# Kernel tuning notes

Measured on AMD Instinct MI355X. Metric: run time of the kernel, lower is better.

The kernel has to match this reference:

```python
import jax, jax.numpy as jnp
import numpy as np

B, H, W, DIM = 8, 64, 64, 256
HEADS, DH = 8, 64
HID = HEADS * DH  # 512
EPS = 1e-5


def setup_inputs() -> dict:
    key = jax.random.key(0)
    k0, k1, k2 = jax.random.split(key, 3)
    return {
        "x": jax.random.normal(k0, (B, H, W, DIM), dtype=jnp.float32),
        "w_qkv": jax.random.normal(k1, (DIM, 3 * HID), dtype=jnp.float32) / np.sqrt(DIM),
        "gn_scale": jnp.ones((HID,), jnp.float32),
        "gn_bias": jnp.zeros((HID,), jnp.float32),
        "w_out": jax.random.normal(k2, (HID, DIM), dtype=jnp.float32) / np.sqrt(HID),
        "b_out": jnp.zeros((DIM,), jnp.float32),
    }


def reference(x, w_qkv, gn_scale, gn_bias, w_out, b_out):
    b, h, w, c = x.shape
    n = h * w
    scale = DH ** -0.5
    # 1x1 conv (no bias) == channel matmul
    qkv = jnp.einsum('bxyc,cf->bxyf', x, w_qkv)
    q, k, v = jnp.split(qkv, 3, axis=-1)
    # 'b x y (h c) -> b h c (x y)'
    to_heads = lambda t: t.reshape(b, n, HEADS, DH).transpose(0, 2, 3, 1)
    q, k, v = map(to_heads, (q, k, v))  # [b, heads, d, n]
    q = jax.nn.softmax(q, axis=-2) * scale  # softmax over feature dim d
    k = jax.nn.softmax(k, axis=-1)          # softmax over token dim n
    context = jnp.einsum('bhdn,bhen->bhde', k, v)   # small d x e context
    out = jnp.einsum('bhde,bhdn->bhen', context, q)  # [b, heads, e, n]
    # 'b h c (x y) -> b x y (h c)'
    out = out.transpose(0, 3, 1, 2).reshape(b, h, w, HID)
    # GroupNorm with 1 group: normalize over (H, W, C) per sample
    mu = out.mean(axis=(1, 2, 3), keepdims=True)
    var = out.var(axis=(1, 2, 3), keepdims=True)
    out = (out - mu) * jax.lax.rsqrt(var + EPS) * gn_scale + gn_bias
    # final 1x1 conv with bias
    return jnp.einsum('bxyf,fc->bxyc', out, w_out) + b_out
```

## Files before the change

### kernel.cpp

```cpp
#include <hip/hip_runtime.h>


typedef unsigned short ushort_t;
typedef __attribute__((ext_vector_type(8))) short short8;
typedef __attribute__((ext_vector_type(4))) float floatx4;

__device__ __forceinline__ float b2f(ushort_t u) {
  unsigned int i = ((unsigned int)u) << 16;
  float f;
  __builtin_memcpy(&f, &i, 4);
  return f;
}
__device__ __forceinline__ ushort_t f2b(float f) {
  unsigned int i;
  __builtin_memcpy(&i, &f, 4);
  unsigned int r = (i + 0x7FFFu + ((i >> 16) & 1u)) >> 16;
  return (ushort_t)r;
}

__device__ __forceinline__ void load_lds16(const ushort_t* g, ushort_t* l) {
  __builtin_amdgcn_global_load_lds(
      (const __attribute__((address_space(1))) unsigned int*)g,
      (__attribute__((address_space(3))) unsigned int*)l, 16, 0, 0);
}

__global__ __launch_bounds__(256) void cast_f32_bf16(
    const float* __restrict__ in, ushort_t* __restrict__ out) {
  long i = ((long)blockIdx.x * 256 + threadIdx.x) * 4;
  float4 v = *(const float4*)(in + i);
  ushort4 o;
  o.x = f2b(v.x);
  o.y = f2b(v.y);
  o.z = f2b(v.z);
  o.w = f2b(v.w);
  *(ushort4*)(out + i) = o;
}

__global__ __launch_bounds__(256) void transpose_f32_bf16(
    const float* __restrict__ in, ushort_t* __restrict__ out, int R, int C,
    const float* __restrict__ scale) {
  __shared__ ushort_t t[32][33];
  int c0 = blockIdx.x * 32, r0 = blockIdx.y * 32;
  int tx = threadIdx.x & 31, ty = threadIdx.x >> 5;
  for (int i = 0; i < 32; i += 8) {
    float s = scale ? scale[r0 + ty + i] : 1.0f;
    t[ty + i][tx] = f2b(in[(long)(r0 + ty + i) * C + c0 + tx] * s);
  }
  __syncthreads();
  for (int i = 0; i < 32; i += 8)
    out[(long)(c0 + ty + i) * R + r0 + tx] = t[tx][ty + i];
}

__global__ __launch_bounds__(64) void prep_gw_kernel(
    const float* __restrict__ gn_scale, const float* __restrict__ gn_bias,
    const float* __restrict__ w_out, const float* __restrict__ b_out,
    float* __restrict__ gw1, float* __restrict__ bias2) {
  int c = blockIdx.x * 64 + threadIdx.x;
  float g1 = 0.f, b2 = 0.f;
  for (int f = 0; f < 512; ++f) {
    float w = w_out[f * 256 + c];
    g1 += gn_scale[f] * w;
    b2 += gn_bias[f] * w;
  }
  gw1[c] = g1;
  bias2[c] = b2 + b_out[c];
}

template <int MODE, bool SWAP>
__global__ __launch_bounds__(256) void gemm_tpl(
    const ushort_t* __restrict__ A, const ushort_t* __restrict__ Bt,
    void* __restrict__ Cv, int M, int K, int F,
    const float* __restrict__ murs, const float* __restrict__ gw1,
    const float* __restrict__ bias2) {
  __shared__ __align__(16) ushort_t As[128][32];
  __shared__ __align__(16) ushort_t Bs[128][32];
  int tid = threadIdx.x;
  long m0 = (long)(SWAP ? blockIdx.y : blockIdx.x) * 128;
  long f0 = (long)(SWAP ? blockIdx.x : blockIdx.y) * 128;
  int wv = tid >> 6, lane = tid & 63;
  int wm = wv & 1, wf = wv >> 1;
  int l15 = lane & 15, quad = lane >> 4;

  floatx4 acc[4][4];
  floatx4 zero = {0.f, 0.f, 0.f, 0.f};
  for (int i = 0; i < 4; i++)
    for (int j = 0; j < 4; j++) acc[i][j] = zero;

  for (int k0 = 0; k0 < K; k0 += 32) {
    __syncthreads();
#pragma unroll
    for (int r = 0; r < 2; ++r) {
      int chunk = r * 256 + tid;
      int row = chunk >> 2;
      int kc = chunk & 3;
      load_lds16(A + (m0 + row) * (long)K + k0 + kc * 8, &As[row][kc * 8]);
      load_lds16(Bt + (f0 + row) * (long)K + k0 + kc * 8, &Bs[row][kc * 8]);
    }
    __syncthreads();
    short8 af[4], bfr[4];
#pragma unroll
    for (int mt = 0; mt < 4; mt++)
      af[mt] = *(const short8*)(&As[wm * 64 + mt * 16 + l15][quad * 8]);
#pragma unroll
    for (int ft = 0; ft < 4; ft++)
      bfr[ft] = *(const short8*)(&Bs[wf * 64 + ft * 16 + l15][quad * 8]);
#pragma unroll
    for (int mt = 0; mt < 4; mt++)
#pragma unroll
      for (int ft = 0; ft < 4; ft++)
        acc[mt][ft] = __builtin_amdgcn_mfma_f32_16x16x32_bf16(
            af[mt], bfr[ft], acc[mt][ft], 0, 0, 0);
  }

  if constexpr (MODE == 0) {
    ushort_t* C = (ushort_t*)Cv;
#pragma unroll
    for (int mt = 0; mt < 4; mt++)
#pragma unroll
      for (int ft = 0; ft < 4; ft++) {
        long col = f0 + wf * 64 + ft * 16 + l15;
#pragma unroll
        for (int r = 0; r < 4; r++) {
          long row = m0 + wm * 64 + mt * 16 + quad * 4 + r;
          C[row * F + col] = f2b(acc[mt][ft][r]);
        }
      }
  } else if constexpr (MODE == 1) {
    ushort_t* C = (ushort_t*)Cv;
    bool isk = (m0 < 512);
#pragma unroll
    for (int mt = 0; mt < 4; mt++)
#pragma unroll
      for (int ft = 0; ft < 4; ft++) {
        long col = f0 + wf * 64 + ft * 16 + l15;
#pragma unroll
        for (int r = 0; r < 4; r++) {
          long row = m0 + wm * 64 + mt * 16 + quad * 4 + r;
          float v = acc[mt][ft][r];
          if (isk) v = __expf(v);
          C[row * F + col] = f2b(v);
        }
      }
  } else {
    float* C = (float*)Cv;
    int b = (int)(m0 >> 12);
    float mu = murs[b * 2], rs = murs[b * 2 + 1];
#pragma unroll
    for (int mt = 0; mt < 4; mt++)
#pragma unroll
      for (int ft = 0; ft < 4; ft++) {
        long col = f0 + wf * 64 + ft * 16 + l15;
        float c1 = bias2[col] - rs * mu * gw1[col];
#pragma unroll
        for (int r = 0; r < 4; r++) {
          long row = m0 + wm * 64 + mt * 16 + quad * 4 + r;
          C[row * F + col] = rs * acc[mt][ft][r] + c1;
        }
      }
  }
}

__global__ __launch_bounds__(256) void ctx_mfma(
    const ushort_t* __restrict__ kvT, float* __restrict__ ctxP,
    float* __restrict__ ksumP) {
  int bh = blockIdx.x, cy = blockIdx.y;
  int b = bh >> 3, h = bh & 7;
  int tid = threadIdx.x, wv = tid >> 6, lane = tid & 63;
  int l15 = lane & 15, quad = lane >> 4;
  __shared__ __align__(16) ushort_t kTs[64 * 128];
  __shared__ __align__(16) ushort_t vTs[64 * 128];
  const ushort_t* kbase = kvT + (long)(h * 64) * 32768 + b * 4096 + cy * 256;
  const ushort_t* vbase = kbase + (long)512 * 32768;

  floatx4 acc[4], acc1;
  floatx4 zero = {0.f, 0.f, 0.f, 0.f};
  for (int i = 0; i < 4; i++) acc[i] = zero;
  acc1 = zero;
  short8 ones;
#pragma unroll
  for (int u = 0; u < 8; ++u) ones[u] = (short)0x3F80;

  int r4 = lane >> 4, c = lane & 15;
  for (int tile = 0; tile < 2; ++tile) {
    __syncthreads();
#pragma unroll
    for (int i = 0; i < 4; ++i) {
      int row = wv * 16 + i * 4 + r4;
      int gc = (c & 8) | ((c ^ row) & 7);
      load_lds16(kbase + (long)row * 32768 + tile * 128 + gc * 8,
                 kTs + (wv * 16 + i * 4) * 128 + lane * 8);
      load_lds16(vbase + (long)row * 32768 + tile * 128 + gc * 8,
                 vTs + (wv * 16 + i * 4) * 128 + lane * 8);
    }
    __syncthreads();
#pragma unroll
    for (int ks = 0; ks < 4; ++ks) {
      int d = wv * 16 + l15;
      int cidx = ks * 4 + quad;
      int sa = (cidx & 8) | ((cidx ^ d) & 7);
      short8 a = *(const short8*)(kTs + d * 128 + sa * 8);
      short8 bf[4];
#pragma unroll
      for (int ft = 0; ft < 4; ++ft) {
        int e = ft * 16 + l15;
        int sb = (cidx & 8) | ((cidx ^ e) & 7);
        bf[ft] = *(const short8*)(vTs + e * 128 + sb * 8);
      }
#pragma unroll
      for (int ft = 0; ft < 4; ++ft)
        acc[ft] = __builtin_amdgcn_mfma_f32_16x16x32_bf16(a, bf[ft], acc[ft],
                                                          0, 0, 0);
      acc1 = __builtin_amdgcn_mfma_f32_16x16x32_bf16(a, ones, acc1, 0, 0, 0);
    }
  }
  float* cb = ctxP + ((long)cy * 64 + bh) * 4096;
#pragma unroll
  for (int ft = 0; ft < 4; ++ft)
#pragma unroll
    for (int r = 0; r < 4; ++r)
      cb[(ft * 16 + l15) * 64 + wv * 16 + quad * 4 + r] = acc[ft][r];
  if (l15 == 0) {
    float* kb = ksumP + ((long)cy * 64 + bh) * 64;
#pragma unroll
    for (int r = 0; r < 4; ++r) kb[wv * 16 + quad * 4 + r] = acc1[r];
  }
}

__global__ __launch_bounds__(256) void reduce_kernel(
    const float* __restrict__ ctxP, const float* __restrict__ ksumP,
    ushort_t* __restrict__ ctxB) {
  int bid = blockIdx.x;
  int bh = bid >> 4;
  int j = (bid & 15) * 256 + threadIdx.x;
  int e = j >> 6, d = j & 63;
  float ks = 0.f;
#pragma unroll
  for (int c = 0; c < 16; ++c) ks += ksumP[((long)c * 64 + bh) * 64 + d];
  float s = 0.f;
#pragma unroll
  for (int c = 0; c < 16; ++c) s += ctxP[((long)c * 64 + bh) * 4096 + j];
  int slot = (d >> 3) ^ (e & 7);
  ctxB[(long)bh * 4096 + e * 64 + slot * 8 + (d & 7)] = f2b(s / ks);
}

__global__ __launch_bounds__(256) void qp_gemm_kernel(
    const ushort_t* __restrict__ q, const ushort_t* __restrict__ ctxB,
    ushort_t* __restrict__ A2, float* __restrict__ gstats) {
  int bh = blockIdx.x, chunk = blockIdx.y;
  int b = bh >> 3, h = bh & 7;
  int tid = threadIdx.x, wv = tid >> 6, lane = tid & 63;
  int l15 = lane & 15, quad = lane >> 4;
  __shared__ __align__(16) ushort_t As[128 * 64];
  __shared__ __align__(16) ushort_t Bs[64 * 64];
  __shared__ float rs[128];
  __shared__ float red[4][2];

  long rowbase = (long)b * 4096 + chunk * 128;

  {
    int tl = lane >> 3;
    int c = lane & 7;
    int j = c ^ tl;
    const ushort_t* g = q + (rowbase + wv * 32 + tl) * 512 + h * 64 + j * 8;
#pragma unroll
    for (int i = 0; i < 4; ++i)
      load_lds16(g + (long)i * 8 * 512, As + (wv * 32 + i * 8) * 64 + lane * 8);
  }
  {
#pragma unroll
    for (int i = 0; i < 2; ++i)
      load_lds16(ctxB + (long)bh * 4096 + (wv * 2 + i) * 512 + lane * 8,
                 Bs + (wv * 2 + i) * 512 + lane * 8);
  }
  __syncthreads();

  {
    int t = tid >> 1, half = tid & 1;
    ushort_t* row = As + t * 64;
    float s = 0.f;
#pragma unroll
    for (int i = 0; i < 4; ++i) {
      int slot = half * 4 + ((i + t) & 3);
      short8 vq = *(const short8*)(row + slot * 8);
      short8 eo;
#pragma unroll
      for (int u = 0; u < 8; ++u) {
        float e = __expf(b2f((ushort_t)vq[u]));
        s += e;
        eo[u] = (short)f2b(e);
      }
      *(short8*)(row + slot * 8) = eo;
    }
    s += __shfl_xor(s, 1);
    if (half == 0) rs[t] = 0.125f / s;
  }
  __syncthreads();

  floatx4 acc[2][4];
  floatx4 zero = {0.f, 0.f, 0.f, 0.f};
  for (int i = 0; i < 2; i++)
    for (int j = 0; j < 4; j++) acc[i][j] = zero;
#pragma unroll
  for (int k0 = 0; k0 < 2; ++k0) {
    short8 af[2], bfr[4];
#pragma unroll
    for (int mt = 0; mt < 2; mt++) {
      int row = wv * 32 + mt * 16 + l15;
      int slot = (k0 * 4 + quad) ^ (row & 7);
      af[mt] = *(const short8*)(As + row * 64 + slot * 8);
    }
#pragma unroll
    for (int ft = 0; ft < 4; ft++) {
      int e = ft * 16 + l15;
      int slot = (k0 * 4 + quad) ^ (e & 7);
      bfr[ft] = *(const short8*)(Bs + e * 64 + slot * 8);
    }
#pragma unroll
    for (int mt = 0; mt < 2; mt++)
#pragma unroll
      for (int ft = 0; ft < 4; ft++)
        acc[mt][ft] = __builtin_amdgcn_mfma_f32_16x16x32_bf16(
            af[mt], bfr[ft], acc[mt][ft], 0, 0, 0);
  }

  float lsum = 0.f, lss = 0.f;
#pragma unroll
  for (int mt = 0; mt < 2; mt++) {
    float rsv[4];
#pragma unroll
    for (int r = 0; r < 4; r++)
      rsv[r] = rs[wv * 32 + mt * 16 + quad * 4 + r];
#pragma unroll
    for (int ft = 0; ft < 4; ft++) {
      int col = h * 64 + ft * 16 + l15;
#pragma unroll
      for (int r = 0; r < 4; r++) {
        long row = rowbase + wv * 32 + mt * 16 + quad * 4 + r;
        float v = acc[mt][ft][r] * rsv[r];
        A2[row * 512 + col] = f2b(v);
        lsum += v;
        lss += v * v;
      }
    }
  }
  for (int o = 32; o > 0; o >>= 1) {
    lsum += __shfl_xor(lsum, o);
    lss += __shfl_xor(lss, o);
  }
  if (lane == 0) {
    red[wv][0] = lsum;
    red[wv][1] = lss;
  }
  __syncthreads();
  if (tid == 0) {
    float a = 0.f, c = 0.f;
    for (int w2 = 0; w2 < 4; w2++) {
      a += red[w2][0];
      c += red[w2][1];
    }
    atomicAdd(&gstats[b * 2], a);
    atomicAdd(&gstats[b * 2 + 1], c);
  }
}

__global__ __launch_bounds__(64) void finalize_murs(
    const float* __restrict__ gstats, float* __restrict__ murs) {
  int tid = threadIdx.x;
  if (tid < 8) {
    float cnt = 4096.f * 512.f;
    float mu = gstats[tid * 2] / cnt;
    float var = gstats[tid * 2 + 1] / cnt - mu * mu;
    murs[tid * 2] = mu;
    murs[tid * 2 + 1] = rsqrtf(var + 1e-5f);
  }
}

extern "C" void kernel_launch(void* const* d_in, const int* in_sizes, int n_in,
                              void* d_out, int out_size, void* d_ws,
                              size_t ws_size, hipStream_t stream) {
  const float* x = (const float*)d_in[0];
  const float* w_qkv = (const float*)d_in[1];
  const float* gn_scale = (const float*)d_in[2];
  const float* gn_bias = (const float*)d_in[3];
  const float* w_out = (const float*)d_in[4];
  const float* b_out = (const float*)d_in[5];
  float* out = (float*)d_out;

  char* w = (char*)d_ws;
  ushort_t* q = (ushort_t*)(w + 0);
  ushort_t* kvT = (ushort_t*)(w + 33554432);
  ushort_t* A2 = (ushort_t*)(w + 100663296);
  float* ctxP = (float*)(w + 134217728);
  float* ksumP = (float*)(w + 150994944);
  ushort_t* xb = (ushort_t*)(w + 167772160);
  ushort_t* wqkvT = (ushort_t*)(w + 184549376);
  ushort_t* w2T = (ushort_t*)(w + 185335808);
  ushort_t* ctxB = (ushort_t*)(w + 185630720);
  float* gstats = (float*)(w + 186679296);
  float* murs = (float*)(w + 186695744);
  float* bias2 = (float*)(w + 186695808);
  float* gw1 = (float*)(w + 186696832);

  hipMemsetAsync(gstats, 0, 64, stream);

  cast_f32_bf16<<<8388608 / 4 / 256, 256, 0, stream>>>(x, xb);
  transpose_f32_bf16<<<dim3(1536 / 32, 256 / 32), 256, 0, stream>>>(
      w_qkv, wqkvT, 256, 1536, nullptr);
  transpose_f32_bf16<<<dim3(256 / 32, 512 / 32), 256, 0, stream>>>(
      w_out, w2T, 512, 256, gn_scale);
  prep_gw_kernel<<<4, 64, 0, stream>>>(gn_scale, gn_bias, w_out, b_out, gw1,
                                       bias2);
  gemm_tpl<0, false><<<dim3(256, 4), 256, 0, stream>>>(
      xb, wqkvT, q, 32768, 256, 512, nullptr, nullptr, nullptr);
  gemm_tpl<1, true><<<dim3(256, 8), 256, 0, stream>>>(
      wqkvT + 512 * 256, xb, kvT, 1024, 256, 32768, nullptr, nullptr, nullptr);
  ctx_mfma<<<dim3(64, 16), 256, 0, stream>>>(kvT, ctxP, ksumP);
  reduce_kernel<<<1024, 256, 0, stream>>>(ctxP, ksumP, ctxB);
  qp_gemm_kernel<<<dim3(64, 32), 256, 0, stream>>>(q, ctxB, A2, gstats);
  finalize_murs<<<1, 64, 0, stream>>>(gstats, murs);
  gemm_tpl<2, false><<<dim3(256, 2), 256, 0, stream>>>(
      A2, w2T, out, 32768, 512, 256, murs, gw1, bias2);
}
```

Before: 270.5 us.

## Fuse Q projection GEMM with softmax and context multiply into one kernel

Removes the separate Q projection GEMM and its bf16 round trip through global memory. A new kernel computes the Q tile from xb and the Q weights, applies exp and the per-head softmax normalisation in registers, stages the probabilities in LDS, and multiplies by the per-head context. It also accumulates the GroupNorm statistics. This saves writing and re-reading a 32 MB intermediate and one launch, at the cost of higher LDS use (about 48 KB) and register pressure, which may lower occupancy.

```diff
diff --git a/kernel.cpp b/kernel.cpp
--- a/kernel.cpp
+++ b/kernel.cpp
@@ -112,20 +112,7 @@
             af[mt], bfr[ft], acc[mt][ft], 0, 0, 0);
   }
 
-  if constexpr (MODE == 0) {
-    ushort_t* C = (ushort_t*)Cv;
-#pragma unroll
-    for (int mt = 0; mt < 4; mt++)
-#pragma unroll
-      for (int ft = 0; ft < 4; ft++) {
-        long col = f0 + wf * 64 + ft * 16 + l15;
-#pragma unroll
-        for (int r = 0; r < 4; r++) {
-          long row = m0 + wm * 64 + mt * 16 + quad * 4 + r;
-          C[row * F + col] = f2b(acc[mt][ft][r]);
-        }
-      }
-  } else if constexpr (MODE == 1) {
+  if constexpr (MODE == 1) {
     ushort_t* C = (ushort_t*)Cv;
     bool isk = (m0 < 512);
 #pragma unroll
@@ -243,120 +230,171 @@
   ctxB[(long)bh * 4096 + e * 64 + slot * 8 + (d & 7)] = f2b(s / ks);
 }
 
-__global__ __launch_bounds__(256) void qp_gemm_kernel(
-    const ushort_t* __restrict__ q, const ushort_t* __restrict__ ctxB,
-    ushort_t* __restrict__ A2, float* __restrict__ gstats) {
-  int bh = blockIdx.x, chunk = blockIdx.y;
-  int b = bh >> 3, h = bh & 7;
-  int tid = threadIdx.x, wv = tid >> 6, lane = tid & 63;
+__global__ __launch_bounds__(256) void qattn_kernel(
+    const ushort_t* __restrict__ xb, const ushort_t* __restrict__ wqT,
+    const ushort_t* __restrict__ ctxB, ushort_t* __restrict__ A2,
+    float* __restrict__ gstats) {
+  __shared__ __align__(16) char lds[49216];
+  ushort_t* As = (ushort_t*)lds;
+  ushort_t* Bs = (ushort_t*)(lds + 8192);
+  ushort_t* P = (ushort_t*)lds;
+  ushort_t* Cs = (ushort_t*)(lds + 32768);
+  float* red = (float*)(lds + 49152);
+
+  int tid = threadIdx.x;
+  int bx = blockIdx.x, by = blockIdx.y;
+  long m0 = (long)bx * 128;
+  long f0 = (long)by * 128;
+  int wv = tid >> 6, lane = tid & 63;
+  int wm = wv & 1, wf = wv >> 1;
   int l15 = lane & 15, quad = lane >> 4;
-  __shared__ __align__(16) ushort_t As[128 * 64];
-  __shared__ __align__(16) ushort_t Bs[64 * 64];
-  __shared__ float rs[128];
-  __shared__ float red[4][2];
-
-  long rowbase = (long)b * 4096 + chunk * 128;
-
-  {
-    int tl = lane >> 3;
-    int c = lane & 7;
-    int j = c ^ tl;
-    const ushort_t* g = q + (rowbase + wv * 32 + tl) * 512 + h * 64 + j * 8;
-#pragma unroll
-    for (int i = 0; i < 4; ++i)
-      load_lds16(g + (long)i * 8 * 512, As + (wv * 32 + i * 8) * 64 + lane * 8);
-  }
-  {
-#pragma unroll
-    for (int i = 0; i < 2; ++i)
-      load_lds16(ctxB + (long)bh * 4096 + (wv * 2 + i) * 512 + lane * 8,
-                 Bs + (wv * 2 + i) * 512 + lane * 8);
-  }
-  __syncthreads();
-
-  {
-    int t = tid >> 1, half = tid & 1;
-    ushort_t* row = As + t * 64;
-    float s = 0.f;
-#pragma unroll
-    for (int i = 0; i < 4; ++i) {
-      int slot = half * 4 + ((i + t) & 3);
-      short8 vq = *(const short8*)(row + slot * 8);
-      short8 eo;
-#pragma unroll
-      for (int u = 0; u < 8; ++u) {
-        float e = __expf(b2f((ushort_t)vq[u]));
-        s += e;
-        eo[u] = (short)f2b(e);
-      }
-      *(short8*)(row + slot * 8) = eo;
-    }
-    s += __shfl_xor(s, 1);
-    if (half == 0) rs[t] = 0.125f / s;
-  }
-  __syncthreads();
-
-  floatx4 acc[2][4];
+  int b = bx >> 5;
+
+  floatx4 acc[4][4];
   floatx4 zero = {0.f, 0.f, 0.f, 0.f};
-  for (int i = 0; i < 2; i++)
+  for (int i = 0; i < 4; i++)
     for (int j = 0; j < 4; j++) acc[i][j] = zero;
-#pragma unroll
-  for (int k0 = 0; k0 < 2; ++k0) {
-    short8 af[2], bfr[4];
-#pragma unroll
-    for (int mt = 0; mt < 2; mt++) {
-      int row = wv * 32 + mt * 16 + l15;
-      int slot = (k0 * 4 + quad) ^ (row & 7);
-      af[mt] = *(const short8*)(As + row * 64 + slot * 8);
-    }
-#pragma unroll
-    for (int ft = 0; ft < 4; ft++) {
-      int e = ft * 16 + l15;
-      int slot = (k0 * 4 + quad) ^ (e & 7);
-      bfr[ft] = *(const short8*)(Bs + e * 64 + slot * 8);
-    }
-#pragma unroll
-    for (int mt = 0; mt < 2; mt++)
+
+  for (int k0 = 0; k0 < 256; k0 += 32) {
+    __syncthreads();
+#pragma unroll
+    for (int r = 0; r < 2; ++r) {
+      int chunk = r * 256 + tid;
+      int row = chunk >> 2;
+      int kc = chunk & 3;
+      load_lds16(xb + (m0 + row) * 256 + k0 + kc * 8, As + row * 32 + kc * 8);
+      load_lds16(wqT + (f0 + row) * 256 + k0 + kc * 8, Bs + row * 32 + kc * 8);
+    }
+    __syncthreads();
+    short8 af[4], bfr[4];
+#pragma unroll
+    for (int mt = 0; mt < 4; mt++)
+      af[mt] = *(const short8*)(As + (wm * 64 + mt * 16 + l15) * 32 + quad * 8);
+#pragma unroll
+    for (int ft = 0; ft < 4; ft++)
+      bfr[ft] =
+          *(const short8*)(Bs + (wf * 64 + ft * 16 + l15) * 32 + quad * 8);
+#pragma unroll
+    for (int mt = 0; mt < 4; mt++)
 #pragma unroll
       for (int ft = 0; ft < 4; ft++)
         acc[mt][ft] = __builtin_amdgcn_mfma_f32_16x16x32_bf16(
             af[mt], bfr[ft], acc[mt][ft], 0, 0, 0);
   }
+  __syncthreads();
+
+  {
+    const ushort_t* cg = ctxB + ((long)(b * 8 + by * 2)) * 4096;
+#pragma unroll
+    for (int i = 0; i < 4; ++i)
+      load_lds16(cg + (i * 4 + wv) * 512 + lane * 8,
+                 Cs + (i * 4 + wv) * 512 + lane * 8);
+  }
+
+  float rs[4][4];
+#pragma unroll
+  for (int mt = 0; mt < 4; mt++)
+#pragma unroll
+    for (int r = 0; r < 4; r++) rs[mt][r] = 0.f;
+#pragma unroll
+  for (int mt = 0; mt < 4; mt++)
+#pragma unroll
+    for (int ft = 0; ft < 4; ft++)
+#pragma unroll
+      for (int r = 0; r < 4; r++) {
+        float e = __expf(acc[mt][ft][r]);
+        acc[mt][ft][r] = e;
+        rs[mt][r] += e;
+      }
+#pragma unroll
+  for (int mt = 0; mt < 4; mt++)
+#pragma unroll
+    for (int r = 0; r < 4; r++) {
+      float t = rs[mt][r];
+      t += __shfl_xor(t, 1);
+      t += __shfl_xor(t, 2);
+      t += __shfl_xor(t, 4);
+      t += __shfl_xor(t, 8);
+      rs[mt][r] = 0.125f / t;
+    }
+
+  {
+    ushort_t* Pw = P + wf * 8192;
+#pragma unroll
+    for (int mt = 0; mt < 4; mt++)
+#pragma unroll
+      for (int ft = 0; ft < 4; ft++) {
+        int d = ft * 16 + l15;
+#pragma unroll
+        for (int r = 0; r < 4; r++) {
+          int row = wm * 64 + mt * 16 + quad * 4 + r;
+          int slot = (d >> 3) ^ (row & 7);
+          Pw[row * 64 + slot * 8 + (d & 7)] = f2b(acc[mt][ft][r]);
+        }
+      }
+  }
+  __syncthreads();
+
+  floatx4 o[4][4];
+  for (int i = 0; i < 4; i++)
+    for (int j = 0; j < 4; j++) o[i][j] = zero;
+  {
+    const ushort_t* Pr = P + wf * 8192;
+    const ushort_t* Cr = Cs + wf * 4096;
+#pragma unroll
+    for (int k0 = 0; k0 < 2; ++k0) {
+      short8 af[4], bfr[4];
+#pragma unroll
+      for (int mt = 0; mt < 4; mt++) {
+        int row = wm * 64 + mt * 16 + l15;
+        int slot = (k0 * 4 + quad) ^ (row & 7);
+        af[mt] = *(const short8*)(Pr + row * 64 + slot * 8);
+      }
+#pragma unroll
+      for (int ft = 0; ft < 4; ft++) {
+        int e = ft * 16 + l15;
+        int slot = (k0 * 4 + quad) ^ (e & 7);
+        bfr[ft] = *(const short8*)(Cr + e * 64 + slot * 8);
+      }
+#pragma unroll
+      for (int mt = 0; mt < 4; mt++)
+#pragma unroll
+        for (int ft = 0; ft < 4; ft++)
+          o[mt][ft] = __builtin_amdgcn_mfma_f32_16x16x32_bf16(af[mt], bfr[ft],
+                                                              o[mt][ft], 0, 0,
+                                                              0);
+    }
+  }
 
   float lsum = 0.f, lss = 0.f;
 #pragma unroll
-  for (int mt = 0; mt < 2; mt++) {
-    float rsv[4];
-#pragma unroll
-    for (int r = 0; r < 4; r++)
-      rsv[r] = rs[wv * 32 + mt * 16 + quad * 4 + r];
+  for (int mt = 0; mt < 4; mt++)
 #pragma unroll
     for (int ft = 0; ft < 4; ft++) {
-      int col = h * 64 + ft * 16 + l15;
+      long col = f0 + wf * 64 + ft * 16 + l15;
 #pragma unroll
       for (int r = 0; r < 4; r++) {
-        long row = rowbase + wv * 32 + mt * 16 + quad * 4 + r;
-        float v = acc[mt][ft][r] * rsv[r];
+        long row = m0 + wm * 64 + mt * 16 + quad * 4 + r;
+        float v = o[mt][ft][r] * rs[mt][r];
         A2[row * 512 + col] = f2b(v);
         lsum += v;
         lss += v * v;
       }
     }
-  }
-  for (int o = 32; o > 0; o >>= 1) {
-    lsum += __shfl_xor(lsum, o);
-    lss += __shfl_xor(lss, o);
+  for (int s = 32; s > 0; s >>= 1) {
+    lsum += __shfl_xor(lsum, s);
+    lss += __shfl_xor(lss, s);
   }
   if (lane == 0) {
-    red[wv][0] = lsum;
-    red[wv][1] = lss;
+    red[wv * 2] = lsum;
+    red[wv * 2 + 1] = lss;
   }
   __syncthreads();
   if (tid == 0) {
     float a = 0.f, c = 0.f;
     for (int w2 = 0; w2 < 4; w2++) {
-      a += red[w2][0];
-      c += red[w2][1];
+      a += red[w2 * 2];
+      c += red[w2 * 2 + 1];
     }
     atomicAdd(&gstats[b * 2], a);
     atomicAdd(&gstats[b * 2 + 1], c);
@@ -387,7 +425,6 @@
   float* out = (float*)d_out;
 
   char* w = (char*)d_ws;
-  ushort_t* q = (ushort_t*)(w + 0);
   ushort_t* kvT = (ushort_t*)(w + 33554432);
   ushort_t* A2 = (ushort_t*)(w + 100663296);
   float* ctxP = (float*)(w + 134217728);
@@ -410,13 +447,11 @@
       w_out, w2T, 512, 256, gn_scale);
   prep_gw_kernel<<<4, 64, 0, stream>>>(gn_scale, gn_bias, w_out, b_out, gw1,
                                        bias2);
-  gemm_tpl<0, false><<<dim3(256, 4), 256, 0, stream>>>(
-      xb, wqkvT, q, 32768, 256, 512, nullptr, nullptr, nullptr);
   gemm_tpl<1, true><<<dim3(256, 8), 256, 0, stream>>>(
       wqkvT + 512 * 256, xb, kvT, 1024, 256, 32768, nullptr, nullptr, nullptr);
   ctx_mfma<<<dim3(64, 16), 256, 0, stream>>>(kvT, ctxP, ksumP);
   reduce_kernel<<<1024, 256, 0, stream>>>(ctxP, ksumP, ctxB);
-  qp_gemm_kernel<<<dim3(64, 32), 256, 0, stream>>>(q, ctxB, A2, gstats);
+  qattn_kernel<<<dim3(256, 4), 256, 0, stream>>>(xb, wqkvT, ctxB, A2, gstats);
   finalize_murs<<<1, 64, 0, stream>>>(gstats, murs);
   gemm_tpl<2, false><<<dim3(256, 2), 256, 0, stream>>>(
       A2, w2T, out, 32768, 512, 256, murs, gw1, bias2);
```

New measurement: 239.3 us. 11.5% less time.
